# Performance work log

Hardware: AMD Instinct MI355X
Metric: run time of the kernel (lower is better)

The kernel has to match this reference:

```python
import jax, jax.numpy as jnp
import numpy as np

N_NODES = 100000
N_EDGES = 1600000
D_IN = 128
D_HID = 128
D_OUT = 40


def _linear_init(key, fan_in, fan_out):
    # torch nn.Linear default: U(-1/sqrt(fan_in), 1/sqrt(fan_in)) for W and b
    kw, kb = jax.random.split(key)
    bound = 1.0 / np.sqrt(fan_in)
    W = jax.random.uniform(kw, (fan_in, fan_out), jnp.float32, -bound, bound)
    b = jax.random.uniform(kb, (fan_out,), jnp.float32, -bound, bound)
    return W, b


def setup_inputs() -> dict:
    key = jax.random.key(0)
    ks = jax.random.split(key, 8)
    x = jax.random.normal(ks[0], (N_NODES, D_IN), jnp.float32)
    edges = jax.random.randint(ks[1], (2, N_EDGES), 0, N_NODES, jnp.int64)
    # layer 0: MLP(128 -> 128 -> 128)
    W1_0, b1_0 = _linear_init(ks[2], D_IN, D_HID)
    W2_0, b2_0 = _linear_init(ks[3], D_HID, D_HID)
    # layer 1: MLP(128 -> 128 -> 128)
    W1_1, b1_1 = _linear_init(ks[4], D_HID, D_HID)
    W2_1, b2_1 = _linear_init(ks[5], D_HID, D_HID)
    # layer 2: MLP(128 -> 128 -> 40)
    W1_2, b1_2 = _linear_init(ks[6], D_HID, D_HID)
    W2_2, b2_2 = _linear_init(ks[7], D_HID, D_OUT)
    eps = jnp.zeros(())  # GINConv train_eps=True initializes eps=0
    return {
        "x": x, "edges": edges,
        "W1_0": W1_0, "b1_0": b1_0, "W2_0": W2_0, "b2_0": b2_0, "eps_0": eps,
        "W1_1": W1_1, "b1_1": b1_1, "W2_1": W2_1, "b2_1": b2_1, "eps_1": eps,
        "W1_2": W1_2, "b1_2": b1_2, "W2_2": W2_2, "b2_2": b2_2, "eps_2": eps,
    }


def _gin_conv(x, src, dst, eps, W1, b1, W2, b2):
    # sum-aggregate neighbor features: out_i = MLP((1+eps)*x_i + sum_{j->i} x_j)
    aggr = jax.ops.segment_sum(x[src], dst, num_segments=x.shape[0])
    h = (1.0 + eps) * x + aggr
    h = jnp.maximum(h @ W1 + b1, 0.0)  # MLP layer 1 + ReLU
    return h @ W2 + b2                  # MLP layer 2


def reference(x, edges,
              W1_0, b1_0, W2_0, b2_0, eps_0,
              W1_1, b1_1, W2_1, b2_1, eps_1,
              W1_2, b1_2, W2_2, b2_2, eps_2):
    src, dst = edges[0], edges[1]
    # dropout is identity at inference (training=False)
    h = jax.nn.relu(_gin_conv(x, src, dst, eps_0, W1_0, b1_0, W2_0, b2_0))
    h = jax.nn.relu(_gin_conv(h, src, dst, eps_1, W1_1, b1_1, W2_1, b2_1))
    o = _gin_conv(h, src, dst, eps_2, W1_2, b1_2, W2_2, b2_2)
    return jax.nn.log_softmax(o, axis=1)
```

## Files before the change

kernel.cpp:

```cpp
#include <hip/hip_runtime.h>
#include <stdint.h>

typedef __attribute__((ext_vector_type(8))) short short8;
typedef __attribute__((ext_vector_type(4))) short short4v;
typedef __attribute__((ext_vector_type(4))) float float4v;

__device__ __forceinline__ float bf2f(unsigned short s) {
    union { unsigned int u; float f; } c; c.u = ((unsigned int)s) << 16; return c.f;
}
__device__ __forceinline__ unsigned short f2bf(float f) {
    union { float f; unsigned int u; } c; c.f = f;
    unsigned int x = c.u;
    unsigned int r = x + 0x7fffu + ((x >> 16) & 1u);
    return (unsigned short)(r >> 16);
}
__device__ __forceinline__ void unpack2(unsigned int u, float& lo, float& hi) {
    union { unsigned int uu; float ff; } a, b;
    a.uu = u << 16;
    b.uu = u & 0xffff0000u;
    lo = a.ff; hi = b.ff;
}

__global__ __launch_bounds__(256) void bs_count(const int* __restrict__ dst, int nE,
                                                int* __restrict__ bucketCnt) {
    __shared__ int c[512];
    int t = threadIdx.x;
    for (int i = t; i < 512; i += 256) c[i] = 0;
    __syncthreads();
    int base = blockIdx.x * 4096;
    for (int i = t; i < 4096; i += 256) {
        int e = base + i;
        if (e < nE) atomicAdd(&c[dst[e] >> 8], 1);
    }
    __syncthreads();
    for (int i = t; i < 512; i += 256)
        if (c[i]) atomicAdd(&bucketCnt[i], c[i]);
}

__global__ __launch_bounds__(512) void bs_scan(const int* __restrict__ bucketCnt,
                                               int* __restrict__ bucketBase,
                                               int* __restrict__ bucketCur,
                                               int* __restrict__ off, int M, int nE) {
    __shared__ int s[512];
    int t = threadIdx.x;
    int v = bucketCnt[t];
    s[t] = v;
    __syncthreads();
    for (int o = 1; o < 512; o <<= 1) {
        int x = (t >= o) ? s[t - o] : 0;
        __syncthreads();
        s[t] += x;
        __syncthreads();
    }
    bucketBase[t] = s[t] - v;
    bucketCur[t] = s[t] - v;
    if (t == 511) bucketBase[512] = s[511];
    if (t == 0) off[M] = nE;
}

__global__ __launch_bounds__(512) void bs_scatter(const int* __restrict__ src,
                                                  const int* __restrict__ dst, int nE,
                                                  int* __restrict__ bucketCur,
                                                  unsigned int* __restrict__ ebuf) {
    __shared__ int cnt[512];
    __shared__ int excl[512];
    __shared__ int chunk[512];
    __shared__ unsigned int buf[4096];
    __shared__ unsigned short bkt[4096];
    int t = threadIdx.x;
    cnt[t] = 0;
    __syncthreads();
    int base = blockIdx.x * 4096;
    int n = nE - base; if (n > 4096) n = 4096;
    unsigned int pk[8]; int bk[8]; int rk[8];
#pragma unroll
    for (int u = 0; u < 8; ++u) {
        int i = t + u * 512;
        if (i < n) {
            int e = base + i;
            int d = dst[e];
            int b = d >> 8;
            bk[u] = b;
            pk[u] = (unsigned int)src[e] | ((unsigned int)(d & 255) << 17);
            rk[u] = atomicAdd(&cnt[b], 1);
        } else bk[u] = -1;
    }
    __syncthreads();
    excl[t] = cnt[t];
    __syncthreads();
    for (int o = 1; o < 512; o <<= 1) {
        int x = (t >= o) ? excl[t - o] : 0;
        __syncthreads();
        excl[t] += x;
        __syncthreads();
    }
    int ex = excl[t] - cnt[t];
    __syncthreads();
    excl[t] = ex;
    if (cnt[t]) chunk[t] = atomicAdd(&bucketCur[t], cnt[t]);
    __syncthreads();
#pragma unroll
    for (int u = 0; u < 8; ++u) {
        if (bk[u] >= 0) {
            int lp = excl[bk[u]] + rk[u];
            buf[lp] = pk[u];
            bkt[lp] = (unsigned short)bk[u];
        }
    }
    __syncthreads();
    for (int i = t; i < n; i += 512) {
        int b = bkt[i];
        ebuf[chunk[b] + (i - excl[b])] = buf[i];
    }
}

__global__ __launch_bounds__(512) void bs_build(const unsigned int* __restrict__ ebuf,
                                                const int* __restrict__ bucketBase,
                                                int* __restrict__ off,
                                                int* __restrict__ esrc, int M) {
    __shared__ int cnt[256];
    __shared__ int excl[256];
    __shared__ int obuf[5120];
    int t = threadIdx.x, b = blockIdx.x;
    int base = bucketBase[b];
    int n = bucketBase[b + 1] - base;
    if (t < 256) cnt[t] = 0;
    __syncthreads();
    unsigned int pk[10]; int dl[10]; int rk[10];
#pragma unroll
    for (int u = 0; u < 10; ++u) {
        int i = t + u * 512;
        if (i < n) {
            unsigned int p = ebuf[base + i];
            pk[u] = p;
            int d = (p >> 17) & 255;
            dl[u] = d;
            rk[u] = atomicAdd(&cnt[d], 1);
        } else dl[u] = -1;
    }
    __syncthreads();
    if (t < 256) excl[t] = cnt[t];
    __syncthreads();
    for (int o = 1; o < 256; o <<= 1) {
        int x = (t < 256 && t >= o) ? excl[t - o] : 0;
        __syncthreads();
        if (t < 256) excl[t] += x;
        __syncthreads();
    }
    if (t < 256) {
        int ex = excl[t] - cnt[t];
        int node = b * 256 + t;
        if (node < M) off[node] = base + ex;
        excl[t] = ex;
    }
    __syncthreads();
#pragma unroll
    for (int u = 0; u < 10; ++u) {
        if (dl[u] >= 0) {
            int lp = excl[dl[u]] + rk[u];
            if (lp < 5120) obuf[lp] = (int)(pk[u] & 0x1FFFF);
        }
    }
    __syncthreads();
    for (int i = t; i < n; i += 512) esrc[base + i] = obuf[i];
}

struct Prep {
    const float* W[6];
    unsigned short* hi[6];
    const float4* xin;
    uint2* xout;
    int n4;
};

__global__ __launch_bounds__(256) void k_prep(Prep p) {
    int b = blockIdx.x;
    if (b < 344) {
        int mat = b >> 6;
        int rel = b - mat * 64;
        int NPAD = (mat == 5) ? 48 : 128;
        int N = (mat == 5) ? 40 : 128;
        int idx = rel * 256 + threadIdx.x;
        if (idx >= NPAD * 128) return;
        int n = idx >> 7, k = idx & 127;
        float w = (n < N) ? p.W[mat][k * N + n] : 0.f;
        p.hi[mat][idx] = f2bf(w);
    } else {
        int i = (b - 344) * 256 + threadIdx.x;
        if (i >= p.n4) return;
        float4 v = p.xin[i];
        uint2 o;
        o.x = ((unsigned int)f2bf(v.y) << 16) | f2bf(v.x);
        o.y = ((unsigned int)f2bf(v.w) << 16) | f2bf(v.z);
        p.xout[i] = o;
    }
}

__device__ __forceinline__ void acc8(uint4 v, float* s) {
    float a, b;
    unpack2(v.x, a, b); s[0] += a; s[1] += b;
    unpack2(v.y, a, b); s[2] += a; s[3] += b;
    unpack2(v.z, a, b); s[4] += a; s[5] += b;
    unpack2(v.w, a, b); s[6] += a; s[7] += b;
}

__global__ __launch_bounds__(256) void k_aggr(const uint4* __restrict__ Hin,
                                              const int* __restrict__ off,
                                              const int* __restrict__ esrc,
                                              const float* __restrict__ epsp,
                                              uint4* __restrict__ Ahi, int M) {
    int w = threadIdx.x >> 6, lane = threadIdx.x & 63;
    int li = lane & 15, q = lane >> 4;
    int node = blockIdx.x * 16 + w * 4 + q;
    if (node >= M) return;
    float ep = 1.0f + epsp[0];
    uint4 ow = Hin[node * 16 + li];
    float s[8] = {0.f, 0.f, 0.f, 0.f, 0.f, 0.f, 0.f, 0.f};
    int i = off[node], e = off[node + 1];
    for (; i + 8 <= e; i += 8) {
        uint4 v[8];
#pragma unroll
        for (int j = 0; j < 8; ++j) v[j] = Hin[esrc[i + j] * 16 + li];
#pragma unroll
        for (int j = 0; j < 8; ++j) acc8(v[j], s);
    }
    if (i < e) {
        int last = e - 1;
        uint4 v[8];
#pragma unroll
        for (int j = 0; j < 8; ++j) {
            int idx = i + j;
            int cl = idx < last ? idx : last;
            v[j] = Hin[esrc[cl] * 16 + li];
        }
#pragma unroll
        for (int j = 0; j < 8; ++j) {
            bool ok = (i + j) < e;
            uint4 u;
            u.x = ok ? v[j].x : 0u;
            u.y = ok ? v[j].y : 0u;
            u.z = ok ? v[j].z : 0u;
            u.w = ok ? v[j].w : 0u;
            acc8(u, s);
        }
    }
    float o[8];
    unpack2(ow.x, o[0], o[1]);
    unpack2(ow.y, o[2], o[3]);
    unpack2(ow.z, o[4], o[5]);
    unpack2(ow.w, o[6], o[7]);
#pragma unroll
    for (int k = 0; k < 8; ++k) s[k] = ep * o[k] + s[k];
    uint4 r;
    r.x = ((unsigned int)f2bf(s[1]) << 16) | f2bf(s[0]);
    r.y = ((unsigned int)f2bf(s[3]) << 16) | f2bf(s[2]);
    r.z = ((unsigned int)f2bf(s[5]) << 16) | f2bf(s[4]);
    r.w = ((unsigned int)f2bf(s[7]) << 16) | f2bf(s[6]);
    Ahi[node * 16 + li] = r;
}

template <int NT2, bool LOGITS>
__global__ __launch_bounds__(256, 4) void k_mlp(const unsigned short* __restrict__ AhiS,
                                                const unsigned short* __restrict__ W1h,
                                                const float* __restrict__ B1,
                                                const unsigned short* __restrict__ W2h,
                                                const float* __restrict__ B2,
                                                unsigned short* __restrict__ HOut,
                                                float* __restrict__ LOut, int M) {
    __shared__ short wbuf[128 * 136];
    int t = threadIdx.x, w = t >> 6, lane = t & 63;
    int lm = lane & 15, lg = lane >> 4;
    int rbase = blockIdx.x * 128;

    for (int i = t * 8; i < 128 * 128; i += 2048) {
        int n = i >> 7, k = i & 127;
        *(short8*)&wbuf[n * 136 + k] = *(const short8*)(W1h + i);
    }
    __syncthreads();

    short4v h2[2][8];
    bool act[2];
#pragma unroll
    for (int t2 = 0; t2 < 2; ++t2) {
        int r0 = rbase + t2 * 64 + w * 16;
        act[t2] = (r0 < M);
        if (act[t2]) {
            const short* Xp = (const short*)AhiS + (r0 + lm) * 128 + lg * 8;
            short8 xf[4];
#pragma unroll
            for (int kb = 0; kb < 4; ++kb) xf[kb] = *(const short8*)(Xp + kb * 32);
            float4v acc1[8];
#pragma unroll
            for (int nt = 0; nt < 8; ++nt) acc1[nt] = (float4v){0.f, 0.f, 0.f, 0.f};
#pragma unroll
            for (int nt = 0; nt < 8; ++nt) {
#pragma unroll
                for (int kb = 0; kb < 4; ++kb) {
                    short8 wf = *(const short8*)&wbuf[(nt * 16 + lm) * 136 + kb * 32 + lg * 8];
                    acc1[nt] = __builtin_amdgcn_mfma_f32_16x16x32_bf16(wf, xf[kb], acc1[nt], 0, 0, 0);
                }
            }
#pragma unroll
            for (int nt = 0; nt < 8; ++nt) {
                float4 b1 = *(const float4*)(B1 + nt * 16 + lg * 4);
                float v0 = acc1[nt][0] + b1.x; v0 = v0 > 0.f ? v0 : 0.f;
                float v1 = acc1[nt][1] + b1.y; v1 = v1 > 0.f ? v1 : 0.f;
                float v2 = acc1[nt][2] + b1.z; v2 = v2 > 0.f ? v2 : 0.f;
                float v3 = acc1[nt][3] + b1.w; v3 = v3 > 0.f ? v3 : 0.f;
                h2[t2][nt] = (short4v){(short)f2bf(v0), (short)f2bf(v1),
                                       (short)f2bf(v2), (short)f2bf(v3)};
            }
        } else {
#pragma unroll
            for (int nt = 0; nt < 8; ++nt) h2[t2][nt] = (short4v){0, 0, 0, 0};
        }
    }

    __syncthreads();
    for (int i = t * 8; i < NT2 * 16 * 128; i += 2048) {
        int n = i >> 7, k = i & 127;
        *(short8*)&wbuf[n * 136 + k] = *(const short8*)(W2h + i);
    }
    __syncthreads();

    float4v acc2[2][NT2];
#pragma unroll
    for (int t2 = 0; t2 < 2; ++t2)
#pragma unroll
        for (int ot = 0; ot < NT2; ++ot) acc2[t2][ot] = (float4v){0.f, 0.f, 0.f, 0.f};
#pragma unroll
    for (int ot = 0; ot < NT2; ++ot) {
#pragma unroll
        for (int nt = 0; nt < 8; ++nt) {
            short4v wf = *(const short4v*)&wbuf[(ot * 16 + lm) * 136 + nt * 16 + lg * 4];
#pragma unroll
            for (int t2 = 0; t2 < 2; ++t2)
                acc2[t2][ot] = __builtin_amdgcn_mfma_f32_16x16x16bf16_1k(wf, h2[t2][nt],
                                                                         acc2[t2][ot], 0, 0, 0);
        }
    }

#pragma unroll
    for (int t2 = 0; t2 < 2; ++t2) {
        if (!act[t2]) continue;
        int row = rbase + t2 * 64 + w * 16 + lm;
        if (!LOGITS) {
#pragma unroll
            for (int ot = 0; ot < NT2; ++ot) {
                float4 b2 = *(const float4*)(B2 + ot * 16 + lg * 4);
                float v0 = acc2[t2][ot][0] + b2.x; v0 = v0 > 0.f ? v0 : 0.f;
                float v1 = acc2[t2][ot][1] + b2.y; v1 = v1 > 0.f ? v1 : 0.f;
                float v2 = acc2[t2][ot][2] + b2.z; v2 = v2 > 0.f ? v2 : 0.f;
                float v3 = acc2[t2][ot][3] + b2.w; v3 = v3 > 0.f ? v3 : 0.f;
                uint2 pk;
                pk.x = ((unsigned int)f2bf(v1) << 16) | f2bf(v0);
                pk.y = ((unsigned int)f2bf(v3) << 16) | f2bf(v2);
                *(uint2*)(HOut + row * 128 + ot * 16 + lg * 4) = pk;
            }
        } else {
            float vv[NT2][4];
#pragma unroll
            for (int ot = 0; ot < NT2; ++ot) {
                int ub = ot * 16 + lg * 4;
                bool valid = ub <= 36;
                float4 b2 = valid ? *(const float4*)(B2 + ub) : (float4){0.f, 0.f, 0.f, 0.f};
                vv[ot][0] = valid ? acc2[t2][ot][0] + b2.x : -1e30f;
                vv[ot][1] = valid ? acc2[t2][ot][1] + b2.y : -1e30f;
                vv[ot][2] = valid ? acc2[t2][ot][2] + b2.z : -1e30f;
                vv[ot][3] = valid ? acc2[t2][ot][3] + b2.w : -1e30f;
            }
            float m = -1e30f;
#pragma unroll
            for (int ot = 0; ot < NT2; ++ot)
#pragma unroll
                for (int r = 0; r < 4; ++r) m = fmaxf(m, vv[ot][r]);
            m = fmaxf(m, __shfl_xor(m, 16, 64));
            m = fmaxf(m, __shfl_xor(m, 32, 64));
            float s = 0.f;
#pragma unroll
            for (int ot = 0; ot < NT2; ++ot)
#pragma unroll
                for (int r = 0; r < 4; ++r)
                    s += (vv[ot][r] > -1e29f) ? expf(vv[ot][r] - m) : 0.f;
            s += __shfl_xor(s, 16, 64);
            s += __shfl_xor(s, 32, 64);
            float ls = m + logf(s);
#pragma unroll
            for (int ot = 0; ot < NT2; ++ot) {
                int ub = ot * 16 + lg * 4;
                if (ub <= 36) {
                    float4 outv = {vv[ot][0] - ls, vv[ot][1] - ls,
                                   vv[ot][2] - ls, vv[ot][3] - ls};
                    *(float4*)(LOut + row * 40 + ub) = outv;
                }
            }
        }
    }
}

extern "C" void kernel_launch(void* const* d_in, const int* in_sizes, int n_in,
                              void* d_out, int out_size, void* d_ws, size_t ws_size,
                              hipStream_t stream) {
    const float* x    = (const float*)d_in[0];
    const int*   edges = (const int*)d_in[1];
    const float* eps0 = (const float*)d_in[6];
    const float* eps1 = (const float*)d_in[11];
    const float* eps2 = (const float*)d_in[16];
    const float* B1[3] = {(const float*)d_in[3], (const float*)d_in[8], (const float*)d_in[13]};
    const float* B2[3] = {(const float*)d_in[5], (const float*)d_in[10], (const float*)d_in[15]};

    int M  = in_sizes[0] / 128;
    int nE = in_sizes[1] / 2;
    const int* e_src = edges;
    const int* e_dst = edges + nE;

    char* ws = (char*)d_ws;
    size_t o = 0;
    auto alloc = [&](size_t bytes) {
        size_t p = o;
        o = (o + bytes + 511) & ~(size_t)511;
        return ws + p;
    };
    int* bucketCnt  = (int*)alloc(512 * 4);
    int* bucketBase = (int*)alloc(513 * 4);
    int* bucketCur  = (int*)alloc(512 * 4);
    int* off  = (int*)alloc((size_t)(M + 1) * 4);
    int* esrc = (int*)alloc((size_t)nE * 4);
    unsigned int* ebuf = (unsigned int*)alloc((size_t)nE * 4);

    Prep pp;
    pp.W[0] = (const float*)d_in[2];  pp.W[1] = (const float*)d_in[4];
    pp.W[2] = (const float*)d_in[7];  pp.W[3] = (const float*)d_in[9];
    pp.W[4] = (const float*)d_in[12]; pp.W[5] = (const float*)d_in[14];
    for (int m = 0; m < 6; ++m) {
        int npad = (m == 5) ? 48 : 128;
        pp.hi[m] = (unsigned short*)alloc((size_t)npad * 128 * 2);
    }
    unsigned short* xb  = (unsigned short*)alloc((size_t)M * 128 * 2);
    unsigned short* Ahi = (unsigned short*)alloc((size_t)M * 128 * 2);
    unsigned short* Hb  = (unsigned short*)alloc((size_t)M * 128 * 2);
    pp.xin = (const float4*)x;
    pp.xout = (uint2*)xb;
    pp.n4 = M * 32;
    (void)ws_size; (void)n_in; (void)out_size;

    hipMemsetAsync(bucketCnt, 0, 512 * 4, stream);
    int nChunk = (nE + 4095) / 4096;
    int nBk = (M + 255) / 256;
    bs_count<<<nChunk, 256, 0, stream>>>(e_dst, nE, bucketCnt);
    bs_scan<<<1, 512, 0, stream>>>(bucketCnt, bucketBase, bucketCur, off, M, nE);
    bs_scatter<<<nChunk, 512, 0, stream>>>(e_src, e_dst, nE, bucketCur, ebuf);
    bs_build<<<nBk, 512, 0, stream>>>(ebuf, bucketBase, off, esrc, M);
    k_prep<<<344 + (pp.n4 + 255) / 256, 256, 0, stream>>>(pp);

    int gA = (M + 15) / 16;
    int gG = (M + 127) / 128;

    k_aggr<<<gA, 256, 0, stream>>>((const uint4*)xb, off, esrc, eps0, (uint4*)Ahi, M);
    k_mlp<8, false><<<gG, 256, 0, stream>>>(Ahi, pp.hi[0], B1[0],
                                            pp.hi[1], B2[0], Hb, nullptr, M);
    k_aggr<<<gA, 256, 0, stream>>>((const uint4*)Hb, off, esrc, eps1, (uint4*)Ahi, M);
    k_mlp<8, false><<<gG, 256, 0, stream>>>(Ahi, pp.hi[2], B1[1],
                                            pp.hi[3], B2[1], Hb, nullptr, M);
    k_aggr<<<gA, 256, 0, stream>>>((const uint4*)Hb, off, esrc, eps2, (uint4*)Ahi, M);
    k_mlp<3, true><<<gG, 256, 0, stream>>>(Ahi, pp.hi[4], B1[2],
                                           pp.hi[5], B2[2], nullptr,
                                           (float*)d_out, M);
}
```

Baseline: 404.2 us.

## Fuse prep and all GIN layers into one persistent cooperative kernel

Replaces the seven separate launches (prep, three aggregation and three MLP kernels) with one cooperative persistent kernel. It grid-strides over tiles and uses grid-wide syncs between phases, so per-launch overhead and tail gaps between kernels go away. The cost is a grid capped at 1024 blocks, which lowers parallelism for the gather-bound aggregation, plus the grid barriers themselves. The MLP phase also reloads weights into LDS for every tile it processes. A fallback path keeps separate launches if cooperative launch is unavailable.

```diff
diff --git a/kernel.cpp b/kernel.cpp
--- a/kernel.cpp
+++ b/kernel.cpp
@@ -1,5 +1,8 @@
 #include <hip/hip_runtime.h>
+#include <hip/hip_cooperative_groups.h>
 #include <stdint.h>
+
+namespace cg = cooperative_groups;
 
 typedef __attribute__((ext_vector_type(8))) short short8;
 typedef __attribute__((ext_vector_type(4))) short short4v;
@@ -165,34 +168,49 @@
     for (int i = t; i < n; i += 512) esrc[base + i] = obuf[i];
 }
 
-struct Prep {
+
+struct LayerArgs {
     const float* W[6];
     unsigned short* hi[6];
     const float4* xin;
     uint2* xout;
     int n4;
+    const int* off;
+    const int* esrc;
+    const float* eps[3];
+    const float* B1[3];
+    const float* B2[3];
+    unsigned short* xb;
+    unsigned short* Ahi;
+    unsigned short* Hb;
+    float* out;
+    int M;
 };
 
-__global__ __launch_bounds__(256) void k_prep(Prep p) {
-    int b = blockIdx.x;
-    if (b < 344) {
+__device__ __forceinline__ void prep_phase(const LayerArgs& a, int nb) {
+    int t = threadIdx.x;
+    for (int b = blockIdx.x; b < 344; b += nb) {
         int mat = b >> 6;
         int rel = b - mat * 64;
         int NPAD = (mat == 5) ? 48 : 128;
         int N = (mat == 5) ? 40 : 128;
-        int idx = rel * 256 + threadIdx.x;
-        if (idx >= NPAD * 128) return;
-        int n = idx >> 7, k = idx & 127;
-        float w = (n < N) ? p.W[mat][k * N + n] : 0.f;
-        p.hi[mat][idx] = f2bf(w);
-    } else {
-        int i = (b - 344) * 256 + threadIdx.x;
-        if (i >= p.n4) return;
-        float4 v = p.xin[i];
-        uint2 o;
-        o.x = ((unsigned int)f2bf(v.y) << 16) | f2bf(v.x);
-        o.y = ((unsigned int)f2bf(v.w) << 16) | f2bf(v.z);
-        p.xout[i] = o;
+        int idx = rel * 256 + t;
+        if (idx < NPAD * 128) {
+            int n = idx >> 7, k = idx & 127;
+            float wv = (n < N) ? a.W[mat][k * N + n] : 0.f;
+            a.hi[mat][idx] = f2bf(wv);
+        }
+    }
+    int xTiles = (a.n4 + 255) >> 8;
+    for (int b = blockIdx.x; b < xTiles; b += nb) {
+        int i = b * 256 + t;
+        if (i < a.n4) {
+            float4 v = a.xin[i];
+            uint2 o;
+            o.x = ((unsigned int)f2bf(v.y) << 16) | f2bf(v.x);
+            o.y = ((unsigned int)f2bf(v.w) << 16) | f2bf(v.z);
+            a.xout[i] = o;
+        }
     }
 }
 
@@ -204,198 +222,257 @@
     unpack2(v.w, a, b); s[6] += a; s[7] += b;
 }
 
-__global__ __launch_bounds__(256) void k_aggr(const uint4* __restrict__ Hin,
-                                              const int* __restrict__ off,
-                                              const int* __restrict__ esrc,
-                                              const float* __restrict__ epsp,
-                                              uint4* __restrict__ Ahi, int M) {
+__device__ __forceinline__ void aggr_phase(const uint4* __restrict__ Hin,
+                                           const int* __restrict__ off,
+                                           const int* __restrict__ esrc,
+                                           float ep,
+                                           uint4* __restrict__ Ahi,
+                                           int M, int nb) {
     int w = threadIdx.x >> 6, lane = threadIdx.x & 63;
     int li = lane & 15, q = lane >> 4;
-    int node = blockIdx.x * 16 + w * 4 + q;
-    if (node >= M) return;
-    float ep = 1.0f + epsp[0];
-    uint4 ow = Hin[node * 16 + li];
-    float s[8] = {0.f, 0.f, 0.f, 0.f, 0.f, 0.f, 0.f, 0.f};
-    int i = off[node], e = off[node + 1];
-    for (; i + 8 <= e; i += 8) {
-        uint4 v[8];
-#pragma unroll
-        for (int j = 0; j < 8; ++j) v[j] = Hin[esrc[i + j] * 16 + li];
-#pragma unroll
-        for (int j = 0; j < 8; ++j) acc8(v[j], s);
-    }
-    if (i < e) {
-        int last = e - 1;
-        uint4 v[8];
-#pragma unroll
-        for (int j = 0; j < 8; ++j) {
-            int idx = i + j;
-            int cl = idx < last ? idx : last;
-            v[j] = Hin[esrc[cl] * 16 + li];
-        }
-#pragma unroll
-        for (int j = 0; j < 8; ++j) {
-            bool ok = (i + j) < e;
-            uint4 u;
-            u.x = ok ? v[j].x : 0u;
-            u.y = ok ? v[j].y : 0u;
-            u.z = ok ? v[j].z : 0u;
-            u.w = ok ? v[j].w : 0u;
-            acc8(u, s);
-        }
-    }
-    float o[8];
-    unpack2(ow.x, o[0], o[1]);
-    unpack2(ow.y, o[2], o[3]);
-    unpack2(ow.z, o[4], o[5]);
-    unpack2(ow.w, o[6], o[7]);
-#pragma unroll
-    for (int k = 0; k < 8; ++k) s[k] = ep * o[k] + s[k];
-    uint4 r;
-    r.x = ((unsigned int)f2bf(s[1]) << 16) | f2bf(s[0]);
-    r.y = ((unsigned int)f2bf(s[3]) << 16) | f2bf(s[2]);
-    r.z = ((unsigned int)f2bf(s[5]) << 16) | f2bf(s[4]);
-    r.w = ((unsigned int)f2bf(s[7]) << 16) | f2bf(s[6]);
-    Ahi[node * 16 + li] = r;
+    int nTiles = (M + 15) >> 4;
+    for (int tile = blockIdx.x; tile < nTiles; tile += nb) {
+        int node = tile * 16 + w * 4 + q;
+        if (node >= M) continue;
+        uint4 ow = Hin[node * 16 + li];
+        float s[8] = {0.f, 0.f, 0.f, 0.f, 0.f, 0.f, 0.f, 0.f};
+        int i = off[node], e = off[node + 1];
+        for (; i + 8 <= e; i += 8) {
+            uint4 v[8];
+#pragma unroll
+            for (int j = 0; j < 8; ++j) v[j] = Hin[esrc[i + j] * 16 + li];
+#pragma unroll
+            for (int j = 0; j < 8; ++j) acc8(v[j], s);
+        }
+        if (i < e) {
+            int last = e - 1;
+            uint4 v[8];
+#pragma unroll
+            for (int j = 0; j < 8; ++j) {
+                int k = i + j;
+                int cl = k < last ? k : last;
+                v[j] = Hin[esrc[cl] * 16 + li];
+            }
+#pragma unroll
+            for (int j = 0; j < 8; ++j) {
+                bool ok = (i + j) < e;
+                uint4 u;
+                u.x = ok ? v[j].x : 0u;
+                u.y = ok ? v[j].y : 0u;
+                u.z = ok ? v[j].z : 0u;
+                u.w = ok ? v[j].w : 0u;
+                acc8(u, s);
+            }
+        }
+        float o[8];
+        unpack2(ow.x, o[0], o[1]);
+        unpack2(ow.y, o[2], o[3]);
+        unpack2(ow.z, o[4], o[5]);
+        unpack2(ow.w, o[6], o[7]);
+#pragma unroll
+        for (int k = 0; k < 8; ++k) s[k] = ep * o[k] + s[k];
+        uint4 r;
+        r.x = ((unsigned int)f2bf(s[1]) << 16) | f2bf(s[0]);
+        r.y = ((unsigned int)f2bf(s[3]) << 16) | f2bf(s[2]);
+        r.z = ((unsigned int)f2bf(s[5]) << 16) | f2bf(s[4]);
+        r.w = ((unsigned int)f2bf(s[7]) << 16) | f2bf(s[6]);
+        Ahi[node * 16 + li] = r;
+    }
 }
 
 template <int NT2, bool LOGITS>
-__global__ __launch_bounds__(256, 4) void k_mlp(const unsigned short* __restrict__ AhiS,
-                                                const unsigned short* __restrict__ W1h,
-                                                const float* __restrict__ B1,
-                                                const unsigned short* __restrict__ W2h,
-                                                const float* __restrict__ B2,
-                                                unsigned short* __restrict__ HOut,
-                                                float* __restrict__ LOut, int M) {
-    __shared__ short wbuf[128 * 136];
+__device__ __forceinline__ void mlp_phase(short* wbuf,
+                                          const unsigned short* __restrict__ AhiS,
+                                          const unsigned short* __restrict__ W1h,
+                                          const float* __restrict__ B1,
+                                          const unsigned short* __restrict__ W2h,
+                                          const float* __restrict__ B2,
+                                          unsigned short* __restrict__ HOut,
+                                          float* __restrict__ LOut, int M, int nb) {
     int t = threadIdx.x, w = t >> 6, lane = t & 63;
     int lm = lane & 15, lg = lane >> 4;
-    int rbase = blockIdx.x * 128;
-
-    for (int i = t * 8; i < 128 * 128; i += 2048) {
-        int n = i >> 7, k = i & 127;
-        *(short8*)&wbuf[n * 136 + k] = *(const short8*)(W1h + i);
-    }
-    __syncthreads();
-
-    short4v h2[2][8];
-    bool act[2];
-#pragma unroll
-    for (int t2 = 0; t2 < 2; ++t2) {
-        int r0 = rbase + t2 * 64 + w * 16;
-        act[t2] = (r0 < M);
-        if (act[t2]) {
-            const short* Xp = (const short*)AhiS + (r0 + lm) * 128 + lg * 8;
-            short8 xf[4];
-#pragma unroll
-            for (int kb = 0; kb < 4; ++kb) xf[kb] = *(const short8*)(Xp + kb * 32);
-            float4v acc1[8];
-#pragma unroll
-            for (int nt = 0; nt < 8; ++nt) acc1[nt] = (float4v){0.f, 0.f, 0.f, 0.f};
+    int nTiles = (M + 127) >> 7;
+    for (int tile = blockIdx.x; tile < nTiles; tile += nb) {
+        int rbase = tile * 128;
+
+#pragma unroll
+        for (int u = 0; u < 8; ++u) {
+            int i = t * 8 + u * 2048;
+            short8 v = *(const short8*)(W1h + i);
+            *(short8*)&wbuf[(i >> 7) * 136 + (i & 127)] = v;
+        }
+        __syncthreads();
+
+        short4v h2[2][8];
+        bool act[2];
+#pragma unroll
+        for (int t2 = 0; t2 < 2; ++t2) {
+            int r0 = rbase + t2 * 64 + w * 16;
+            act[t2] = (r0 < M);
+            if (act[t2]) {
+                const short* Xp = (const short*)AhiS + (r0 + lm) * 128 + lg * 8;
+                short8 xf[4];
+#pragma unroll
+                for (int kb = 0; kb < 4; ++kb) xf[kb] = *(const short8*)(Xp + kb * 32);
+                float4v acc1[8];
+#pragma unroll
+                for (int nt = 0; nt < 8; ++nt) acc1[nt] = (float4v){0.f, 0.f, 0.f, 0.f};
+#pragma unroll
+                for (int nt = 0; nt < 8; ++nt) {
+#pragma unroll
+                    for (int kb = 0; kb < 4; ++kb) {
+                        short8 wf = *(const short8*)&wbuf[(nt * 16 + lm) * 136 + kb * 32 + lg * 8];
+                        acc1[nt] = __builtin_amdgcn_mfma_f32_16x16x32_bf16(wf, xf[kb], acc1[nt], 0, 0, 0);
+                    }
+                }
+#pragma unroll
+                for (int nt = 0; nt < 8; ++nt) {
+                    float4 b1 = *(const float4*)(B1 + nt * 16 + lg * 4);
+                    float v0 = acc1[nt][0] + b1.x; v0 = v0 > 0.f ? v0 : 0.f;
+                    float v1 = acc1[nt][1] + b1.y; v1 = v1 > 0.f ? v1 : 0.f;
+                    float v2 = acc1[nt][2] + b1.z; v2 = v2 > 0.f ? v2 : 0.f;
+                    float v3 = acc1[nt][3] + b1.w; v3 = v3 > 0.f ? v3 : 0.f;
+                    h2[t2][nt] = (short4v){(short)f2bf(v0), (short)f2bf(v1),
+                                           (short)f2bf(v2), (short)f2bf(v3)};
+                }
+            } else {
+#pragma unroll
+                for (int nt = 0; nt < 8; ++nt) h2[t2][nt] = (short4v){0, 0, 0, 0};
+            }
+        }
+
+        __syncthreads();
+        constexpr int W2CH = (NT2 * 16 * 128) / 2048;
+#pragma unroll
+        for (int u = 0; u < W2CH; ++u) {
+            int i = t * 8 + u * 2048;
+            short8 v = *(const short8*)(W2h + i);
+            *(short8*)&wbuf[(i >> 7) * 136 + (i & 127)] = v;
+        }
+        __syncthreads();
+
+        float4v acc2[2][NT2];
+#pragma unroll
+        for (int t2 = 0; t2 < 2; ++t2)
+#pragma unroll
+            for (int ot = 0; ot < NT2; ++ot) acc2[t2][ot] = (float4v){0.f, 0.f, 0.f, 0.f};
+#pragma unroll
+        for (int ot = 0; ot < NT2; ++ot) {
 #pragma unroll
             for (int nt = 0; nt < 8; ++nt) {
-#pragma unroll
-                for (int kb = 0; kb < 4; ++kb) {
-                    short8 wf = *(const short8*)&wbuf[(nt * 16 + lm) * 136 + kb * 32 + lg * 8];
-                    acc1[nt] = __builtin_amdgcn_mfma_f32_16x16x32_bf16(wf, xf[kb], acc1[nt], 0, 0, 0);
+                short4v wf = *(const short4v*)&wbuf[(ot * 16 + lm) * 136 + nt * 16 + lg * 4];
+#pragma unroll
+                for (int t2 = 0; t2 < 2; ++t2)
+                    acc2[t2][ot] = __builtin_amdgcn_mfma_f32_16x16x16bf16_1k(wf, h2[t2][nt],
+                                                                             acc2[t2][ot], 0, 0, 0);
+            }
+        }
+
+#pragma unroll
+        for (int t2 = 0; t2 < 2; ++t2) {
+            if (!act[t2]) continue;
+            int row = rbase + t2 * 64 + w * 16 + lm;
+            if (!LOGITS) {
+#pragma unroll
+                for (int ot = 0; ot < NT2; ++ot) {
+                    float4 b2 = *(const float4*)(B2 + ot * 16 + lg * 4);
+                    float v0 = acc2[t2][ot][0] + b2.x; v0 = v0 > 0.f ? v0 : 0.f;
+                    float v1 = acc2[t2][ot][1] + b2.y; v1 = v1 > 0.f ? v1 : 0.f;
+                    float v2 = acc2[t2][ot][2] + b2.z; v2 = v2 > 0.f ? v2 : 0.f;
+                    float v3 = acc2[t2][ot][3] + b2.w; v3 = v3 > 0.f ? v3 : 0.f;
+                    uint2 pk;
+                    pk.x = ((unsigned int)f2bf(v1) << 16) | f2bf(v0);
+                    pk.y = ((unsigned int)f2bf(v3) << 16) | f2bf(v2);
+                    *(uint2*)(HOut + row * 128 + ot * 16 + lg * 4) = pk;
+                }
+            } else {
+                float vv[NT2][4];
+#pragma unroll
+                for (int ot = 0; ot < NT2; ++ot) {
+                    int ub = ot * 16 + lg * 4;
+                    bool valid = ub <= 36;
+                    float4 b2 = valid ? *(const float4*)(B2 + ub) : (float4){0.f, 0.f, 0.f, 0.f};
+                    vv[ot][0] = valid ? acc2[t2][ot][0] + b2.x : -1e30f;
+                    vv[ot][1] = valid ? acc2[t2][ot][1] + b2.y : -1e30f;
+                    vv[ot][2] = valid ? acc2[t2][ot][2] + b2.z : -1e30f;
+                    vv[ot][3] = valid ? acc2[t2][ot][3] + b2.w : -1e30f;
+                }
+                float m = -1e30f;
+#pragma unroll
+                for (int ot = 0; ot < NT2; ++ot)
+#pragma unroll
+                    for (int r = 0; r < 4; ++r) m = fmaxf(m, vv[ot][r]);
+                m = fmaxf(m, __shfl_xor(m, 16, 64));
+                m = fmaxf(m, __shfl_xor(m, 32, 64));
+                float s = 0.f;
+#pragma unroll
+                for (int ot = 0; ot < NT2; ++ot)
+#pragma unroll
+                    for (int r = 0; r < 4; ++r)
+                        s += (vv[ot][r] > -1e29f) ? expf(vv[ot][r] - m) : 0.f;
+                s += __shfl_xor(s, 16, 64);
+                s += __shfl_xor(s, 32, 64);
+                float ls = m + logf(s);
+#pragma unroll
+                for (int ot = 0; ot < NT2; ++ot) {
+                    int ub = ot * 16 + lg * 4;
+                    if (ub <= 36) {
+                        float4 outv = {vv[ot][0] - ls, vv[ot][1] - ls,
+                                       vv[ot][2] - ls, vv[ot][3] - ls};
+                        *(float4*)(LOut + row * 40 + ub) = outv;
+                    }
                 }
             }
-#pragma unroll
-            for (int nt = 0; nt < 8; ++nt) {
-                float4 b1 = *(const float4*)(B1 + nt * 16 + lg * 4);
-                float v0 = acc1[nt][0] + b1.x; v0 = v0 > 0.f ? v0 : 0.f;
-                float v1 = acc1[nt][1] + b1.y; v1 = v1 > 0.f ? v1 : 0.f;
-                float v2 = acc1[nt][2] + b1.z; v2 = v2 > 0.f ? v2 : 0.f;
-                float v3 = acc1[nt][3] + b1.w; v3 = v3 > 0.f ? v3 : 0.f;
-                h2[t2][nt] = (short4v){(short)f2bf(v0), (short)f2bf(v1),
-                                       (short)f2bf(v2), (short)f2bf(v3)};
-            }
+        }
+    }
+}
+
+__global__ __launch_bounds__(256, 4) void k_layers(LayerArgs a) {
+    cg::grid_group grid = cg::this_grid();
+    __shared__ short wbuf[128 * 136];
+    int nb = gridDim.x;
+
+    prep_phase(a, nb);
+    grid.sync();
+
+    for (int L = 0; L < 3; ++L) {
+        const unsigned short* Hin = (L == 0) ? a.xb : a.Hb;
+        float ep = 1.0f + a.eps[L][0];
+        aggr_phase((const uint4*)Hin, a.off, a.esrc, ep, (uint4*)a.Ahi, a.M, nb);
+        grid.sync();
+        if (L < 2) {
+            mlp_phase<8, false>(wbuf, a.Ahi, a.hi[2 * L], a.B1[L], a.hi[2 * L + 1],
+                                a.B2[L], a.Hb, nullptr, a.M, nb);
+            grid.sync();
         } else {
-#pragma unroll
-            for (int nt = 0; nt < 8; ++nt) h2[t2][nt] = (short4v){0, 0, 0, 0};
-        }
-    }
-
-    __syncthreads();
-    for (int i = t * 8; i < NT2 * 16 * 128; i += 2048) {
-        int n = i >> 7, k = i & 127;
-        *(short8*)&wbuf[n * 136 + k] = *(const short8*)(W2h + i);
-    }
-    __syncthreads();
-
-    float4v acc2[2][NT2];
-#pragma unroll
-    for (int t2 = 0; t2 < 2; ++t2)
-#pragma unroll
-        for (int ot = 0; ot < NT2; ++ot) acc2[t2][ot] = (float4v){0.f, 0.f, 0.f, 0.f};
-#pragma unroll
-    for (int ot = 0; ot < NT2; ++ot) {
-#pragma unroll
-        for (int nt = 0; nt < 8; ++nt) {
-            short4v wf = *(const short4v*)&wbuf[(ot * 16 + lm) * 136 + nt * 16 + lg * 4];
-#pragma unroll
-            for (int t2 = 0; t2 < 2; ++t2)
-                acc2[t2][ot] = __builtin_amdgcn_mfma_f32_16x16x16bf16_1k(wf, h2[t2][nt],
-                                                                         acc2[t2][ot], 0, 0, 0);
-        }
-    }
-
-#pragma unroll
-    for (int t2 = 0; t2 < 2; ++t2) {
-        if (!act[t2]) continue;
-        int row = rbase + t2 * 64 + w * 16 + lm;
-        if (!LOGITS) {
-#pragma unroll
-            for (int ot = 0; ot < NT2; ++ot) {
-                float4 b2 = *(const float4*)(B2 + ot * 16 + lg * 4);
-                float v0 = acc2[t2][ot][0] + b2.x; v0 = v0 > 0.f ? v0 : 0.f;
-                float v1 = acc2[t2][ot][1] + b2.y; v1 = v1 > 0.f ? v1 : 0.f;
-                float v2 = acc2[t2][ot][2] + b2.z; v2 = v2 > 0.f ? v2 : 0.f;
-                float v3 = acc2[t2][ot][3] + b2.w; v3 = v3 > 0.f ? v3 : 0.f;
-                uint2 pk;
-                pk.x = ((unsigned int)f2bf(v1) << 16) | f2bf(v0);
-                pk.y = ((unsigned int)f2bf(v3) << 16) | f2bf(v2);
-                *(uint2*)(HOut + row * 128 + ot * 16 + lg * 4) = pk;
-            }
-        } else {
-            float vv[NT2][4];
-#pragma unroll
-            for (int ot = 0; ot < NT2; ++ot) {
-                int ub = ot * 16 + lg * 4;
-                bool valid = ub <= 36;
-                float4 b2 = valid ? *(const float4*)(B2 + ub) : (float4){0.f, 0.f, 0.f, 0.f};
-                vv[ot][0] = valid ? acc2[t2][ot][0] + b2.x : -1e30f;
-                vv[ot][1] = valid ? acc2[t2][ot][1] + b2.y : -1e30f;
-                vv[ot][2] = valid ? acc2[t2][ot][2] + b2.z : -1e30f;
-                vv[ot][3] = valid ? acc2[t2][ot][3] + b2.w : -1e30f;
-            }
-            float m = -1e30f;
-#pragma unroll
-            for (int ot = 0; ot < NT2; ++ot)
-#pragma unroll
-                for (int r = 0; r < 4; ++r) m = fmaxf(m, vv[ot][r]);
-            m = fmaxf(m, __shfl_xor(m, 16, 64));
-            m = fmaxf(m, __shfl_xor(m, 32, 64));
-            float s = 0.f;
-#pragma unroll
-            for (int ot = 0; ot < NT2; ++ot)
-#pragma unroll
-                for (int r = 0; r < 4; ++r)
-                    s += (vv[ot][r] > -1e29f) ? expf(vv[ot][r] - m) : 0.f;
-            s += __shfl_xor(s, 16, 64);
-            s += __shfl_xor(s, 32, 64);
-            float ls = m + logf(s);
-#pragma unroll
-            for (int ot = 0; ot < NT2; ++ot) {
-                int ub = ot * 16 + lg * 4;
-                if (ub <= 36) {
-                    float4 outv = {vv[ot][0] - ls, vv[ot][1] - ls,
-                                   vv[ot][2] - ls, vv[ot][3] - ls};
-                    *(float4*)(LOut + row * 40 + ub) = outv;
-                }
-            }
-        }
-    }
+            mlp_phase<3, true>(wbuf, a.Ahi, a.hi[4], a.B1[2], a.hi[5],
+                               a.B2[2], nullptr, a.out, a.M, nb);
+        }
+    }
+}
+
+__global__ __launch_bounds__(256) void k_prep_sep(LayerArgs a) {
+    prep_phase(a, gridDim.x);
+}
+
+__global__ __launch_bounds__(256) void k_aggr_sep(const uint4* __restrict__ Hin,
+                                                  const int* __restrict__ off,
+                                                  const int* __restrict__ esrc,
+                                                  const float* __restrict__ epsp,
+                                                  uint4* __restrict__ Ahi, int M) {
+    aggr_phase(Hin, off, esrc, 1.0f + epsp[0], Ahi, M, gridDim.x);
+}
+
+template <int NT2, bool LOGITS>
+__global__ __launch_bounds__(256, 2) void k_mlp_sep(const unsigned short* __restrict__ AhiS,
+                                                    const unsigned short* __restrict__ W1h,
+                                                    const float* __restrict__ B1,
+                                                    const unsigned short* __restrict__ W2h,
+                                                    const float* __restrict__ B2,
+                                                    unsigned short* __restrict__ HOut,
+                                                    float* __restrict__ LOut, int M) {
+    __shared__ short wbuf[128 * 136];
+    mlp_phase<NT2, LOGITS>(wbuf, AhiS, W1h, B1, W2h, B2, HOut, LOut, M, gridDim.x);
 }
 
 extern "C" void kernel_launch(void* const* d_in, const int* in_sizes, int n_in,
@@ -403,11 +480,6 @@
                               hipStream_t stream) {
     const float* x    = (const float*)d_in[0];
     const int*   edges = (const int*)d_in[1];
-    const float* eps0 = (const float*)d_in[6];
-    const float* eps1 = (const float*)d_in[11];
-    const float* eps2 = (const float*)d_in[16];
-    const float* B1[3] = {(const float*)d_in[3], (const float*)d_in[8], (const float*)d_in[13]};
-    const float* B2[3] = {(const float*)d_in[5], (const float*)d_in[10], (const float*)d_in[15]};
 
     int M  = in_sizes[0] / 128;
     int nE = in_sizes[1] / 2;
@@ -428,20 +500,34 @@
     int* esrc = (int*)alloc((size_t)nE * 4);
     unsigned int* ebuf = (unsigned int*)alloc((size_t)nE * 4);
 
-    Prep pp;
-    pp.W[0] = (const float*)d_in[2];  pp.W[1] = (const float*)d_in[4];
-    pp.W[2] = (const float*)d_in[7];  pp.W[3] = (const float*)d_in[9];
-    pp.W[4] = (const float*)d_in[12]; pp.W[5] = (const float*)d_in[14];
+    LayerArgs la;
+    la.W[0] = (const float*)d_in[2];  la.W[1] = (const float*)d_in[4];
+    la.W[2] = (const float*)d_in[7];  la.W[3] = (const float*)d_in[9];
+    la.W[4] = (const float*)d_in[12]; la.W[5] = (const float*)d_in[14];
     for (int m = 0; m < 6; ++m) {
         int npad = (m == 5) ? 48 : 128;
-        pp.hi[m] = (unsigned short*)alloc((size_t)npad * 128 * 2);
+        la.hi[m] = (unsigned short*)alloc((size_t)npad * 128 * 2);
     }
     unsigned short* xb  = (unsigned short*)alloc((size_t)M * 128 * 2);
     unsigned short* Ahi = (unsigned short*)alloc((size_t)M * 128 * 2);
     unsigned short* Hb  = (unsigned short*)alloc((size_t)M * 128 * 2);
-    pp.xin = (const float4*)x;
-    pp.xout = (uint2*)xb;
-    pp.n4 = M * 32;
+    la.xin = (const float4*)x;
+    la.xout = (uint2*)xb;
+    la.n4 = M * 32;
+    la.off = off;
+    la.esrc = esrc;
+    la.eps[0] = (const float*)d_in[6];
+    la.eps[1] = (const float*)d_in[11];
+    la.eps[2] = (const float*)d_in[16];
+    la.B1[0] = (const float*)d_in[3];  la.B1[1] = (const float*)d_in[8];
+    la.B1[2] = (const float*)d_in[13];
+    la.B2[0] = (const float*)d_in[5];  la.B2[1] = (const float*)d_in[10];
+    la.B2[2] = (const float*)d_in[15];
+    la.xb = xb;
+    la.Ahi = Ahi;
+    la.Hb = Hb;
+    la.out = (float*)d_out;
+    la.M = M;
     (void)ws_size; (void)n_in; (void)out_size;
 
     hipMemsetAsync(bucketCnt, 0, 512 * 4, stream);
@@ -451,19 +537,36 @@
     bs_scan<<<1, 512, 0, stream>>>(bucketCnt, bucketBase, bucketCur, off, M, nE);
     bs_scatter<<<nChunk, 512, 0, stream>>>(e_src, e_dst, nE, bucketCur, ebuf);
     bs_build<<<nBk, 512, 0, stream>>>(ebuf, bucketBase, off, esrc, M);
-    k_prep<<<344 + (pp.n4 + 255) / 256, 256, 0, stream>>>(pp);
-
-    int gA = (M + 15) / 16;
-    int gG = (M + 127) / 128;
-
-    k_aggr<<<gA, 256, 0, stream>>>((const uint4*)xb, off, esrc, eps0, (uint4*)Ahi, M);
-    k_mlp<8, false><<<gG, 256, 0, stream>>>(Ahi, pp.hi[0], B1[0],
-                                            pp.hi[1], B2[0], Hb, nullptr, M);
-    k_aggr<<<gA, 256, 0, stream>>>((const uint4*)Hb, off, esrc, eps1, (uint4*)Ahi, M);
-    k_mlp<8, false><<<gG, 256, 0, stream>>>(Ahi, pp.hi[2], B1[1],
-                                            pp.hi[3], B2[1], Hb, nullptr, M);
-    k_aggr<<<gA, 256, 0, stream>>>((const uint4*)Hb, off, esrc, eps2, (uint4*)Ahi, M);
-    k_mlp<3, true><<<gG, 256, 0, stream>>>(Ahi, pp.hi[4], B1[2],
-                                           pp.hi[5], B2[2], nullptr,
-                                           (float*)d_out, M);
-}
+
+    bool coop = false;
+    int occ = 0;
+    if (hipOccupancyMaxActiveBlocksPerMultiprocessor(&occ, k_layers, 256, 0)
+            == hipSuccess && occ >= 3) {
+        int grid = occ * 256;
+        if (grid > 1024) grid = 1024;
+        void* args[] = { &la };
+        if (hipLaunchCooperativeKernel((const void*)k_layers, dim3(grid),
+                                       dim3(256), args, 0, stream) == hipSuccess)
+            coop = true;
+    }
+
+    if (!coop) {
+        int gP = 391;
+        int gA = (M + 15) / 16;
+        int gG = (M + 127) / 128;
+        k_prep_sep<<<gP, 256, 0, stream>>>(la);
+        k_aggr_sep<<<gA, 256, 0, stream>>>((const uint4*)xb, off, esrc, la.eps[0],
+                                           (uint4*)Ahi, M);
+        k_mlp_sep<8, false><<<gG, 256, 0, stream>>>(Ahi, la.hi[0], la.B1[0],
+                                                    la.hi[1], la.B2[0], Hb, nullptr, M);
+        k_aggr_sep<<<gA, 256, 0, stream>>>((const uint4*)Hb, off, esrc, la.eps[1],
+                                           (uint4*)Ahi, M);
+        k_mlp_sep<8, false><<<gG, 256, 0, stream>>>(Ahi, la.hi[2], la.B1[1],
+                                                    la.hi[3], la.B2[1], Hb, nullptr, M);
+        k_aggr_sep<<<gA, 256, 0, stream>>>((const uint4*)Hb, off, esrc, la.eps[2],
+                                           (uint4*)Ahi, M);
+        k_mlp_sep<3, true><<<gG, 256, 0, stream>>>(Ahi, la.hi[4], la.B1[2],
+                                                   la.hi[5], la.B2[2], nullptr,
+                                                   (float*)d_out, M);
+    }
+}
```

After: 430.1 us. +6.4%, slower.
